# Performance work log

Measured on AMD Instinct MI355X. Metric: run time of the kernel, lower is better.

The kernel has to match this reference:

```python
import jax, jax.numpy as jnp
import numpy as np

N_NODES = 50000
NEG_SLOPE = 0.2  # PyG GATConv default
EPS = 1e-16      # PyG softmax eps


def gat_conv(x, src, dst, W, a_s, a_d, b, n_nodes):
    """One PyG-style GATConv layer (concat heads). a_s/a_d: [H, C]."""
    H, C = a_s.shape
    h = (x @ W).reshape(n_nodes, H, C)                   # [N, H, C]
    al_s = jnp.sum(h * a_s[None], axis=-1)               # [N, H]
    al_d = jnp.sum(h * a_d[None], axis=-1)               # [N, H]
    e = jax.nn.leaky_relu(al_s[src] + al_d[dst], NEG_SLOPE)  # [E, H]
    # segment softmax over incoming edges of each destination node
    m = jax.ops.segment_max(e, dst, num_segments=n_nodes)
    m = jnp.where(jnp.isfinite(m), m, 0.0)
    ex = jnp.exp(e - m[dst])
    denom = jax.ops.segment_sum(ex, dst, num_segments=n_nodes)
    alpha = ex / (denom[dst] + EPS)                       # [E, H]
    out = jax.ops.segment_sum(alpha[:, :, None] * h[src], dst, num_segments=n_nodes)
    return out.reshape(n_nodes, H * C) + b                # concat heads + bias


def setup_inputs() -> dict:
    key = jax.random.key(0)
    ks = jax.random.split(key, 16)
    s = 0.05
    return {
        "x": jax.random.normal(ks[0], (N_NODES, 256), jnp.float32),
        "edge_index": jax.random.randint(ks[1], (2, 800000), 0, N_NODES, jnp.int64),
        "W1": jax.random.normal(ks[2], (256, 256), jnp.float32) * s,
        "as1": jax.random.normal(ks[3], (4, 64), jnp.float32) * s,
        "ad1": jax.random.normal(ks[4], (4, 64), jnp.float32) * s,
        "b1": jnp.zeros((256,), jnp.float32),
        "W2": jax.random.normal(ks[5], (256, 256), jnp.float32) * s,
        "as2": jax.random.normal(ks[6], (4, 64), jnp.float32) * s,
        "ad2": jax.random.normal(ks[7], (4, 64), jnp.float32) * s,
        "b2": jnp.zeros((256,), jnp.float32),
        "W3": jax.random.normal(ks[8], (256, 128), jnp.float32) * s,
        "as3": jax.random.normal(ks[9], (1, 128), jnp.float32) * s,
        "ad3": jax.random.normal(ks[10], (1, 128), jnp.float32) * s,
        "b3": jnp.zeros((128,), jnp.float32),
    }


def reference(x, edge_index, W1, as1, ad1, b1, W2, as2, ad2, b2, W3, as3, ad3, b3):
    n = x.shape[0]
    loop = jnp.arange(n, dtype=edge_index.dtype)
    src = jnp.concatenate([edge_index[0], loop])  # add_self_loops=True (PyG default)
    dst = jnp.concatenate([edge_index[1], loop])
    # F.dropout(p=0.6, training=False) -> identity in eval
    h = gat_conv(x, src, dst, W1, as1, ad1, b1, n)
    h = jax.nn.elu(h)  # gnn_act='elu'
    h = gat_conv(h, src, dst, W2, as2, ad2, b2, n)
    h = jax.nn.elu(h)
    h = gat_conv(h, src, dst, W3, as3, ad3, b3, n)
    return h
```

## Files before the change

### kernel.cpp

```cpp
#include <hip/hip_runtime.h>
#include <math.h>


#define NEG_SLOPE 0.2f
#define EPS_SM 1e-16f

typedef _Float16 half8 __attribute__((ext_vector_type(8)));
typedef _Float16 half4v __attribute__((ext_vector_type(4)));
typedef _Float16 half2v __attribute__((ext_vector_type(2)));
typedef float f32x4 __attribute__((ext_vector_type(4)));

__device__ __forceinline__ float wave_allred_sum(float v) {
#pragma unroll
    for (int o = 32; o > 0; o >>= 1) v += __shfl_xor(v, o, 64);
    return v;
}
__device__ __forceinline__ float4 lrelu4(float4 v) {
    v.x = (v.x < 0.f) ? NEG_SLOPE * v.x : v.x;
    v.y = (v.y < 0.f) ? NEG_SLOPE * v.y : v.y;
    v.z = (v.z < 0.f) ? NEG_SLOPE * v.z : v.z;
    v.w = (v.w < 0.f) ? NEG_SLOPE * v.w : v.w;
    return v;
}

__global__ void build_fused(const int* __restrict__ ei, int E, int N, int nbE,
                            int* __restrict__ cnt, int* __restrict__ csr,
                            const float* __restrict__ W1,
                            const float* __restrict__ W2,
                            const float* __restrict__ W3,
                            const float* __restrict__ as1, const float* __restrict__ ad1,
                            const float* __restrict__ as2, const float* __restrict__ ad2,
                            const float* __restrict__ as3, const float* __restrict__ ad3,
                            _Float16* __restrict__ o1,
                            _Float16* __restrict__ o2,
                            _Float16* __restrict__ o3) {
    const int b = blockIdx.x;
    if (b < nbE) {
        int e = b * 256 + threadIdx.x;
        int ET = E + N;
        if (e >= ET) return;
        int src, dst;
        if (e < E) { src = ei[e]; dst = ei[E + e]; }
        else       { src = dst = e - E; }
        int slot = atomicAdd(&cnt[dst], 1);
        if (slot < 128) csr[(dst << 7) + slot] = src;
        return;
    }
    int i = (b - nbE) * 256 + threadIdx.x;
    if (i < 65536) {
        int n = i >> 8, k = i & 255;
        o1[i] = (_Float16)W1[(size_t)k * 256 + n];
    } else if (i < 131072) {
        int s = i - 65536; int n = s >> 8, k = s & 255;
        o2[s] = (_Float16)W2[(size_t)k * 256 + n];
    } else if (i < 163840) {
        int s = i - 131072; int n = s >> 8, k = s & 255;
        o3[s] = (_Float16)W3[(size_t)k * 128 + n];
    } else if (i < 163840 + 4096) {
        int t = i - 163840; int j = t >> 8, k = t & 255;
        float acc = 0.f;
        if (j < 8) {
            int h = j & 3;
            const float* a = ((j < 4) ? as1 : ad1) + h * 64;
            const float* wr = W1 + (size_t)k * 256 + h * 64;
            for (int c = 0; c < 64; ++c) acc += wr[c] * a[c];
        }
        o1[65536 + t] = (_Float16)acc;
    } else if (i < 163840 + 8192) {
        int t = i - 163840 - 4096; int j = t >> 8, k = t & 255;
        float acc = 0.f;
        if (j < 8) {
            int h = j & 3;
            const float* a = ((j < 4) ? as2 : ad2) + h * 64;
            const float* wr = W2 + (size_t)k * 256 + h * 64;
            for (int c = 0; c < 64; ++c) acc += wr[c] * a[c];
        }
        o2[65536 + t] = (_Float16)acc;
    } else if (i < 163840 + 12288) {
        int t = i - 163840 - 8192; int j = t >> 8, k = t & 255;
        float acc = 0.f;
        if (j < 2) {
            const float* a = (j == 0) ? as3 : ad3;
            const float* wr = W3 + (size_t)k * 128;
            for (int c = 0; c < 128; ++c) acc += wr[c] * a[c];
        }
        o3[32768 + t] = (_Float16)acc;
    }
}

template <bool AF32>
__global__ __launch_bounds__(256) void gemm_wide64(
    const void* __restrict__ Ain, const _Float16* __restrict__ Bt,
    _Float16* __restrict__ C,
    float* __restrict__ als, float* __restrict__ ald, int M) {
    const int K = 256, N = 256;
    __shared__ _Float16 As[2][64][40], Bs[2][272][40];
    const int bm = blockIdx.x * 64;
    const int tid = threadIdx.x;
    const int w = tid >> 6, lane = tid & 63;
    const int wn = w * 64;
    const int l16 = lane & 15, q = lane >> 4;
    const int kq = q * 8;
    const int arow = tid >> 2, ak = (tid & 3) * 8;
    const int brow = tid;
    const int agrow = bm + arow;
    const int NT = K >> 5;

    f32x4 acc[4][4], acce[4];
#pragma unroll
    for (int i = 0; i < 4; ++i) {
#pragma unroll
        for (int j = 0; j < 4; ++j) acc[i][j] = (f32x4){0.f, 0.f, 0.f, 0.f};
        acce[i] = (f32x4){0.f, 0.f, 0.f, 0.f};
    }

    half8 ra, rb0, rb1, rb2, rb3, rbe;
    auto LOAD = [&](int kt) {
        if constexpr (AF32) {
            const float* Af = (const float*)Ain;
            float4 v0, v1;
            if (agrow < M) {
                const float4* ap = (const float4*)(Af + (size_t)agrow * K + kt + ak);
                v0 = ap[0]; v1 = ap[1];
            } else {
                v0 = v1 = make_float4(0.f, 0.f, 0.f, 0.f);
            }
            ra[0] = (_Float16)v0.x; ra[1] = (_Float16)v0.y;
            ra[2] = (_Float16)v0.z; ra[3] = (_Float16)v0.w;
            ra[4] = (_Float16)v1.x; ra[5] = (_Float16)v1.y;
            ra[6] = (_Float16)v1.z; ra[7] = (_Float16)v1.w;
        } else {
            const _Float16* Ah = (const _Float16*)Ain;
            if (agrow < M) {
                ra = *(const half8*)(Ah + (size_t)agrow * K + kt + ak);
            } else {
                ra = (half8)(_Float16)0;
            }
        }
        const half8* bp = (const half8*)(Bt + (size_t)brow * K + kt);
        rb0 = bp[0]; rb1 = bp[1]; rb2 = bp[2]; rb3 = bp[3];
        if (tid < 64) {
            int er = tid >> 2, ek = (tid & 3) * 8;
            rbe = *(const half8*)(Bt + (size_t)(256 + er) * K + kt + ek);
        }
    };
    auto STORE = [&](int nb) {
        *(half8*)&As[nb][arow][ak]  = ra;
        *(half8*)&Bs[nb][brow][0]   = rb0;
        *(half8*)&Bs[nb][brow][8]   = rb1;
        *(half8*)&Bs[nb][brow][16]  = rb2;
        *(half8*)&Bs[nb][brow][24]  = rb3;
        if (tid < 64) {
            int er = tid >> 2, ek = (tid & 3) * 8;
            *(half8*)&Bs[nb][256 + er][ek] = rbe;
        }
    };

    LOAD(0);
    STORE(0);
    int cur = 0;
    for (int kb = 0; kb < NT; ++kb) {
        const bool more = (kb + 1) < NT;
        if (more) LOAD((kb + 1) * 32);
        __syncthreads();
        half8 a[4], b[4];
#pragma unroll
        for (int t = 0; t < 4; ++t) {
            a[t] = *(const half8*)&As[cur][t * 16 + l16][kq];
            b[t] = *(const half8*)&Bs[cur][wn + t * 16 + l16][kq];
        }
#pragma unroll
        for (int i = 0; i < 4; ++i)
#pragma unroll
            for (int j = 0; j < 4; ++j)
                acc[i][j] = __builtin_amdgcn_mfma_f32_16x16x32_f16(
                    a[i], b[j], acc[i][j], 0, 0, 0);
        if (w == 0) {
            half8 be = *(const half8*)&Bs[cur][256 + l16][kq];
#pragma unroll
            for (int i = 0; i < 4; ++i)
                acce[i] = __builtin_amdgcn_mfma_f32_16x16x32_f16(
                    a[i], be, acce[i], 0, 0, 0);
        }
        if (more) STORE(cur ^ 1);
        cur ^= 1;
    }

#pragma unroll
    for (int i = 0; i < 4; ++i) {
#pragma unroll
        for (int r = 0; r < 4; ++r) {
            int orow = bm + i * 16 + q * 4 + r;
            if (orow < M) {
                _Float16* cp = C + (size_t)orow * N + wn + l16;
                cp[0]  = (_Float16)acc[i][0][r];
                cp[16] = (_Float16)acc[i][1][r];
                cp[32] = (_Float16)acc[i][2][r];
                cp[48] = (_Float16)acc[i][3][r];
            }
        }
    }
    if (w == 0) {
#pragma unroll
        for (int i = 0; i < 4; ++i) {
#pragma unroll
            for (int r = 0; r < 4; ++r) {
                int orow = bm + i * 16 + q * 4 + r;
                if (orow < M) {
                    float c = acce[i][r];
                    if (l16 < 4)      als[orow * 4 + l16] = c;
                    else if (l16 < 8) ald[orow * 4 + (l16 - 4)] = c;
                }
            }
        }
    }
}

__global__ __launch_bounds__(256) void gemm_f16_l3(
    const _Float16* __restrict__ Ain, const _Float16* __restrict__ Bt,
    _Float16* __restrict__ C,
    float* __restrict__ als, float* __restrict__ ald,
    int M, int N, int K) {
    __shared__ _Float16 As[2][128][40], Bs[2][144][40];
    const int bm = blockIdx.y * 128;
    const int tid = threadIdx.x;
    const int w = tid >> 6, lane = tid & 63;
    const int wm = (w >> 1) * 64, wn = (w & 1) * 64;
    const int l16 = lane & 15, q = lane >> 4;
    const int kq = q * 8;
    const int sr = tid >> 1;
    const int sk = (tid & 1) * 16;
    const int row = bm + sr;
    const int NT = K >> 5;

    f32x4 acc[4][4], acce[4];
#pragma unroll
    for (int i = 0; i < 4; ++i) {
#pragma unroll
        for (int j = 0; j < 4; ++j) acc[i][j] = (f32x4){0.f, 0.f, 0.f, 0.f};
        acce[i] = (f32x4){0.f, 0.f, 0.f, 0.f};
    }

    half8 ra0, ra1, rb0, rb1, rbe;
    auto LOAD = [&](int kt) {
        if (row < M) {
            const half8* ap = (const half8*)(Ain + (size_t)row * K + kt + sk);
            ra0 = ap[0]; ra1 = ap[1];
        } else {
            ra0 = (half8)(_Float16)0; ra1 = (half8)(_Float16)0;
        }
        const half8* bp = (const half8*)(Bt + (size_t)sr * K + kt + sk);
        rb0 = bp[0]; rb1 = bp[1];
        if (tid < 64) {
            int er = tid >> 2, ek = (tid & 3) * 8;
            rbe = *(const half8*)(Bt + (size_t)(128 + er) * K + kt + ek);
        }
    };
    auto STORE = [&](int nb) {
        *(half8*)&As[nb][sr][sk]     = ra0;
        *(half8*)&As[nb][sr][sk + 8] = ra1;
        *(half8*)&Bs[nb][sr][sk]     = rb0;
        *(half8*)&Bs[nb][sr][sk + 8] = rb1;
        if (tid < 64) {
            int er = tid >> 2, ek = (tid & 3) * 8;
            *(half8*)&Bs[nb][128 + er][ek] = rbe;
        }
    };

    LOAD(0);
    STORE(0);
    int cur = 0;
    for (int kb = 0; kb < NT; ++kb) {
        const bool more = (kb + 1) < NT;
        if (more) LOAD((kb + 1) * 32);
        __syncthreads();
        half8 a[4], b[4];
#pragma unroll
        for (int t = 0; t < 4; ++t) {
            a[t] = *(const half8*)&As[cur][wm + t * 16 + l16][kq];
            b[t] = *(const half8*)&Bs[cur][wn + t * 16 + l16][kq];
        }
#pragma unroll
        for (int i = 0; i < 4; ++i)
#pragma unroll
            for (int j = 0; j < 4; ++j)
                acc[i][j] = __builtin_amdgcn_mfma_f32_16x16x32_f16(
                    a[i], b[j], acc[i][j], 0, 0, 0);
        if (wn == 0) {
            half8 be = *(const half8*)&Bs[cur][128 + l16][kq];
#pragma unroll
            for (int i = 0; i < 4; ++i)
                acce[i] = __builtin_amdgcn_mfma_f32_16x16x32_f16(
                    a[i], be, acce[i], 0, 0, 0);
        }
        if (more) STORE(cur ^ 1);
        cur ^= 1;
    }

#pragma unroll
    for (int i = 0; i < 4; ++i) {
#pragma unroll
        for (int r = 0; r < 4; ++r) {
            int orow = bm + wm + i * 16 + q * 4 + r;
            if (orow < M) {
                _Float16* cp = C + (size_t)orow * N + wn + l16;
                cp[0]  = (_Float16)acc[i][0][r];
                cp[16] = (_Float16)acc[i][1][r];
                cp[32] = (_Float16)acc[i][2][r];
                cp[48] = (_Float16)acc[i][3][r];
            }
        }
    }
    if (wn == 0) {
#pragma unroll
        for (int i = 0; i < 4; ++i) {
#pragma unroll
            for (int r = 0; r < 4; ++r) {
                int orow = bm + wm + i * 16 + q * 4 + r;
                if (orow < M) {
                    float c = acce[i][r];
                    if (l16 == 0)      als[orow] = c;
                    else if (l16 == 1) ald[orow] = c;
                }
            }
        }
    }
}

template <bool ACT>
__global__ __launch_bounds__(256) void aggregate_h4_f16(
    const _Float16* __restrict__ h, const float4* __restrict__ als4,
    const float4* __restrict__ ald4, const int* __restrict__ cnt,
    const int* __restrict__ csr, const float* __restrict__ bias,
    _Float16* __restrict__ out, int Nn) {
    const int tid = threadIdx.x;
    const int w = tid >> 6;
    const int l = tid & 63;
    const int n = blockIdx.x * 4 + w;
    __shared__ float s_alpha[4][64][4];
    __shared__ int s_src[4][64];
    if (n >= Nn) return;

    const int base = n << 7;
    const int deg = min(cnt[n], 128);
    const float4 adv = ald4[n];
    const int head = l >> 4;

    float4 acc = make_float4(0.f, 0.f, 0.f, 0.f);
    float4 den = make_float4(0.f, 0.f, 0.f, 0.f);
    for (int c0 = 0; c0 < deg; c0 += 64) {
        const int cl = min(64, deg - c0);
        if (l < cl) {
            int s = csr[base + c0 + l];
            float4 a = als4[s];
            float4 sc = lrelu4(make_float4(a.x + adv.x, a.y + adv.y,
                                           a.z + adv.z, a.w + adv.w));
            float4 ex = make_float4(__expf(sc.x), __expf(sc.y),
                                    __expf(sc.z), __expf(sc.w));
            *(float4*)&s_alpha[w][l][0] = ex;
            s_src[w][l] = s;
            den.x += ex.x; den.y += ex.y; den.z += ex.z; den.w += ex.w;
        }
        int e = 0;
        for (; e + 4 <= cl; e += 4) {
            int s0 = s_src[w][e + 0], s1 = s_src[w][e + 1];
            int s2 = s_src[w][e + 2], s3 = s_src[w][e + 3];
            float a0 = s_alpha[w][e + 0][head];
            float a1 = s_alpha[w][e + 1][head];
            float a2 = s_alpha[w][e + 2][head];
            float a3 = s_alpha[w][e + 3][head];
            half4v hv0 = *(const half4v*)(h + (size_t)s0 * 256 + l * 4);
            half4v hv1 = *(const half4v*)(h + (size_t)s1 * 256 + l * 4);
            half4v hv2 = *(const half4v*)(h + (size_t)s2 * 256 + l * 4);
            half4v hv3 = *(const half4v*)(h + (size_t)s3 * 256 + l * 4);
            acc.x = fmaf(a0, (float)hv0[0], acc.x);
            acc.y = fmaf(a0, (float)hv0[1], acc.y);
            acc.z = fmaf(a0, (float)hv0[2], acc.z);
            acc.w = fmaf(a0, (float)hv0[3], acc.w);
            acc.x = fmaf(a1, (float)hv1[0], acc.x);
            acc.y = fmaf(a1, (float)hv1[1], acc.y);
            acc.z = fmaf(a1, (float)hv1[2], acc.z);
            acc.w = fmaf(a1, (float)hv1[3], acc.w);
            acc.x = fmaf(a2, (float)hv2[0], acc.x);
            acc.y = fmaf(a2, (float)hv2[1], acc.y);
            acc.z = fmaf(a2, (float)hv2[2], acc.z);
            acc.w = fmaf(a2, (float)hv2[3], acc.w);
            acc.x = fmaf(a3, (float)hv3[0], acc.x);
            acc.y = fmaf(a3, (float)hv3[1], acc.y);
            acc.z = fmaf(a3, (float)hv3[2], acc.z);
            acc.w = fmaf(a3, (float)hv3[3], acc.w);
        }
        for (; e < cl; ++e) {
            int s0 = s_src[w][e];
            float a0 = s_alpha[w][e][head];
            half4v hv0 = *(const half4v*)(h + (size_t)s0 * 256 + l * 4);
            acc.x = fmaf(a0, (float)hv0[0], acc.x);
            acc.y = fmaf(a0, (float)hv0[1], acc.y);
            acc.z = fmaf(a0, (float)hv0[2], acc.z);
            acc.w = fmaf(a0, (float)hv0[3], acc.w);
        }
    }
    den.x = wave_allred_sum(den.x); den.y = wave_allred_sum(den.y);
    den.z = wave_allred_sum(den.z); den.w = wave_allred_sum(den.w);
    float d = (head == 0) ? den.x : (head == 1) ? den.y
             : (head == 2) ? den.z : den.w;
    const float rc = 1.f / (d + EPS_SM);

    float4 bv = *(const float4*)(bias + l * 4);
    float4 r = make_float4(acc.x * rc + bv.x, acc.y * rc + bv.y,
                           acc.z * rc + bv.z, acc.w * rc + bv.w);
    if (ACT) {
        r.x = (r.x > 0.f) ? r.x : expm1f(r.x);
        r.y = (r.y > 0.f) ? r.y : expm1f(r.y);
        r.z = (r.z > 0.f) ? r.z : expm1f(r.z);
        r.w = (r.w > 0.f) ? r.w : expm1f(r.w);
    }
    half4v ov = {(_Float16)r.x, (_Float16)r.y, (_Float16)r.z, (_Float16)r.w};
    *(half4v*)(out + (size_t)n * 256 + l * 4) = ov;
}

__global__ __launch_bounds__(256) void aggregate_h1_f16(
    const _Float16* __restrict__ h, const float* __restrict__ als,
    const float* __restrict__ ald, const int* __restrict__ cnt,
    const int* __restrict__ csr, const float* __restrict__ bias,
    float* __restrict__ out, int Nn) {
    const int tid = threadIdx.x;
    const int w = tid >> 6;
    const int l = tid & 63;
    const int n = blockIdx.x * 4 + w;
    __shared__ float s_alpha[4][64];
    __shared__ int s_src[4][64];
    if (n >= Nn) return;

    const int base = n << 7;
    const int deg = min(cnt[n], 128);
    const float ad_n = ald[n];

    float2 acc = make_float2(0.f, 0.f);
    float den = 0.f;
    for (int c0 = 0; c0 < deg; c0 += 64) {
        const int cl = min(64, deg - c0);
        if (l < cl) {
            int s = csr[base + c0 + l];
            float sc = als[s] + ad_n;
            sc = (sc < 0.f) ? NEG_SLOPE * sc : sc;
            float ex = __expf(sc);
            s_alpha[w][l] = ex;
            s_src[w][l] = s;
            den += ex;
        }
        int e = 0;
        for (; e + 4 <= cl; e += 4) {
            int s0 = s_src[w][e + 0], s1 = s_src[w][e + 1];
            int s2 = s_src[w][e + 2], s3 = s_src[w][e + 3];
            float a0 = s_alpha[w][e + 0], a1 = s_alpha[w][e + 1];
            float a2 = s_alpha[w][e + 2], a3 = s_alpha[w][e + 3];
            half2v v0 = *(const half2v*)(h + (size_t)s0 * 128 + l * 2);
            half2v v1 = *(const half2v*)(h + (size_t)s1 * 128 + l * 2);
            half2v v2 = *(const half2v*)(h + (size_t)s2 * 128 + l * 2);
            half2v v3 = *(const half2v*)(h + (size_t)s3 * 128 + l * 2);
            acc.x = fmaf(a0, (float)v0[0], acc.x); acc.y = fmaf(a0, (float)v0[1], acc.y);
            acc.x = fmaf(a1, (float)v1[0], acc.x); acc.y = fmaf(a1, (float)v1[1], acc.y);
            acc.x = fmaf(a2, (float)v2[0], acc.x); acc.y = fmaf(a2, (float)v2[1], acc.y);
            acc.x = fmaf(a3, (float)v3[0], acc.x); acc.y = fmaf(a3, (float)v3[1], acc.y);
        }
        for (; e < cl; ++e) {
            int s0 = s_src[w][e];
            float a0 = s_alpha[w][e];
            half2v v0 = *(const half2v*)(h + (size_t)s0 * 128 + l * 2);
            acc.x = fmaf(a0, (float)v0[0], acc.x); acc.y = fmaf(a0, (float)v0[1], acc.y);
        }
    }
    den = wave_allred_sum(den);
    const float rc = 1.f / (den + EPS_SM);
    float2 r = make_float2(acc.x * rc + bias[l * 2],
                           acc.y * rc + bias[l * 2 + 1]);
    *(float2*)(out + (size_t)n * 128 + l * 2) = r;
}

extern "C" void kernel_launch(void* const* d_in, const int* in_sizes, int n_in,
                              void* d_out, int out_size, void* d_ws,
                              size_t ws_size, hipStream_t stream) {
    const float* x   = (const float*)d_in[0];
    const int*   ei  = (const int*)d_in[1];
    const float* W1  = (const float*)d_in[2];
    const float* as1 = (const float*)d_in[3];
    const float* ad1 = (const float*)d_in[4];
    const float* b1  = (const float*)d_in[5];
    const float* W2  = (const float*)d_in[6];
    const float* as2 = (const float*)d_in[7];
    const float* ad2 = (const float*)d_in[8];
    const float* b2  = (const float*)d_in[9];
    const float* W3  = (const float*)d_in[10];
    const float* as3 = (const float*)d_in[11];
    const float* ad3 = (const float*)d_in[12];
    const float* b3  = (const float*)d_in[13];

    const int Nn = in_sizes[0] / 256;
    const int E  = in_sizes[1] / 2;
    const int ET = E + Nn;

    char* p = (char*)d_ws;
    _Float16* bufA = (_Float16*)p; p += (size_t)Nn * 256 * 2;
    _Float16* bufB = (_Float16*)p; p += (size_t)Nn * 256 * 2;
    float* als  = (float*)p; p += (size_t)Nn * 4 * 4;
    float* ald  = (float*)p; p += (size_t)Nn * 4 * 4;
    int* cnt  = (int*)p; p += (size_t)Nn * 4;
    int* csr  = (int*)p; p += (size_t)Nn * 128 * 4;
    p = (char*)(((uintptr_t)p + 15) & ~(uintptr_t)15);
    _Float16* wt1 = (_Float16*)p; p += 272 * 256 * 2;
    _Float16* wt2 = (_Float16*)p; p += 272 * 256 * 2;
    _Float16* wt3 = (_Float16*)p; p += 144 * 256 * 2;

    hipMemsetAsync(cnt, 0, (size_t)Nn * sizeof(int), stream);
    const int nbE = (ET + 255) / 256;
    const int nbW = (163840 + 12288 + 255) / 256;
    build_fused<<<nbE + nbW, 256, 0, stream>>>(
        ei, E, Nn, nbE, cnt, csr,
        W1, W2, W3, as1, ad1, as2, ad2, as3, ad3, wt1, wt2, wt3);

    const int gm64 = (Nn + 63) / 64;
    const int gm   = (Nn + 127) / 128;
    const int ga   = (Nn + 3) / 4;

    gemm_wide64<true><<<gm64, 256, 0, stream>>>(
        x, wt1, bufB, als, ald, Nn);
    aggregate_h4_f16<true><<<ga, 256, 0, stream>>>(
        bufB, (const float4*)als, (const float4*)ald, cnt, csr, b1, bufA, Nn);

    gemm_wide64<false><<<gm64, 256, 0, stream>>>(
        bufA, wt2, bufB, als, ald, Nn);
    aggregate_h4_f16<true><<<ga, 256, 0, stream>>>(
        bufB, (const float4*)als, (const float4*)ald, cnt, csr, b2, bufA, Nn);

    gemm_f16_l3<<<dim3(1, gm), 256, 0, stream>>>(
        bufA, wt3, bufB, als, ald, Nn, 128, 256);
    aggregate_h1_f16<<<ga, 256, 0, stream>>>(
        bufB, als, ald, cnt, csr, b3, (float*)d_out, Nn);
}
```

Measured before the change: 392.8 us.

## Fold CSR build into first GEMM launch and zero counters in prep kernel

Replaces the memset with a counter-zeroing section in the weight-prep kernel. The edge-bucketing atomics move out of that kernel and into extra blocks appended to the layer-1 GEMM grid, so CSR construction runs concurrently with the first GEMM. This removes one API call and hides the atomic scatter behind GEMM compute. The cost is that GEMM blocks share the device with the atomic-heavy blocks, and the build blocks still reserve the GEMM's shared-memory footprint, which may lower occupancy for them.

```diff
diff --git a/kernel.cpp b/kernel.cpp
--- a/kernel.cpp
+++ b/kernel.cpp
@@ -23,30 +23,23 @@
     return v;
 }
 
-__global__ void build_fused(const int* __restrict__ ei, int E, int N, int nbE,
-                            int* __restrict__ cnt, int* __restrict__ csr,
-                            const float* __restrict__ W1,
-                            const float* __restrict__ W2,
-                            const float* __restrict__ W3,
-                            const float* __restrict__ as1, const float* __restrict__ ad1,
-                            const float* __restrict__ as2, const float* __restrict__ ad2,
-                            const float* __restrict__ as3, const float* __restrict__ ad3,
-                            _Float16* __restrict__ o1,
-                            _Float16* __restrict__ o2,
-                            _Float16* __restrict__ o3) {
+__global__ void prep(int* __restrict__ cnt, int Nn, int nbZ,
+                     const float* __restrict__ W1,
+                     const float* __restrict__ W2,
+                     const float* __restrict__ W3,
+                     const float* __restrict__ as1, const float* __restrict__ ad1,
+                     const float* __restrict__ as2, const float* __restrict__ ad2,
+                     const float* __restrict__ as3, const float* __restrict__ ad3,
+                     _Float16* __restrict__ o1,
+                     _Float16* __restrict__ o2,
+                     _Float16* __restrict__ o3) {
     const int b = blockIdx.x;
-    if (b < nbE) {
-        int e = b * 256 + threadIdx.x;
-        int ET = E + N;
-        if (e >= ET) return;
-        int src, dst;
-        if (e < E) { src = ei[e]; dst = ei[E + e]; }
-        else       { src = dst = e - E; }
-        int slot = atomicAdd(&cnt[dst], 1);
-        if (slot < 128) csr[(dst << 7) + slot] = src;
+    if (b < nbZ) {
+        int i = b * 256 + threadIdx.x;
+        if (i < Nn) cnt[i] = 0;
         return;
     }
-    int i = (b - nbE) * 256 + threadIdx.x;
+    int i = (b - nbZ) * 256 + threadIdx.x;
     if (i < 65536) {
         int n = i >> 8, k = i & 255;
         o1[i] = (_Float16)W1[(size_t)k * 256 + n];
@@ -88,13 +81,29 @@
     }
 }
 
-template <bool AF32>
+template <bool AF32, bool BUILD>
 __global__ __launch_bounds__(256) void gemm_wide64(
     const void* __restrict__ Ain, const _Float16* __restrict__ Bt,
     _Float16* __restrict__ C,
-    float* __restrict__ als, float* __restrict__ ald, int M) {
+    float* __restrict__ als, float* __restrict__ ald, int M,
+    const int* __restrict__ ei, int E,
+    int* __restrict__ cnt, int* __restrict__ csr, int nbG) {
     const int K = 256, N = 256;
     __shared__ _Float16 As[2][64][40], Bs[2][272][40];
+    if constexpr (BUILD) {
+        if (blockIdx.x >= nbG) {
+            int e = (blockIdx.x - nbG) * 256 + threadIdx.x;
+            int ET = E + M;
+            if (e < ET) {
+                int src, dst;
+                if (e < E) { src = ei[e]; dst = ei[E + e]; }
+                else       { src = dst = e - E; }
+                int slot = atomicAdd(&cnt[dst], 1);
+                if (slot < 128) csr[(dst << 7) + slot] = src;
+            }
+            return;
+        }
+    }
     const int bm = blockIdx.x * 64;
     const int tid = threadIdx.x;
     const int w = tid >> 6, lane = tid & 63;
@@ -512,24 +521,23 @@
     _Float16* wt2 = (_Float16*)p; p += 272 * 256 * 2;
     _Float16* wt3 = (_Float16*)p; p += 144 * 256 * 2;
 
-    hipMemsetAsync(cnt, 0, (size_t)Nn * sizeof(int), stream);
+    const int nbZ = (Nn + 255) / 256;
+    const int nbW = (163840 + 12288 + 255) / 256;
     const int nbE = (ET + 255) / 256;
-    const int nbW = (163840 + 12288 + 255) / 256;
-    build_fused<<<nbE + nbW, 256, 0, stream>>>(
-        ei, E, Nn, nbE, cnt, csr,
-        W1, W2, W3, as1, ad1, as2, ad2, as3, ad3, wt1, wt2, wt3);
-
     const int gm64 = (Nn + 63) / 64;
     const int gm   = (Nn + 127) / 128;
     const int ga   = (Nn + 3) / 4;
 
-    gemm_wide64<true><<<gm64, 256, 0, stream>>>(
-        x, wt1, bufB, als, ald, Nn);
+    prep<<<nbZ + nbW, 256, 0, stream>>>(
+        cnt, Nn, nbZ, W1, W2, W3, as1, ad1, as2, ad2, as3, ad3, wt1, wt2, wt3);
+
+    gemm_wide64<true, true><<<gm64 + nbE, 256, 0, stream>>>(
+        x, wt1, bufB, als, ald, Nn, ei, E, cnt, csr, gm64);
     aggregate_h4_f16<true><<<ga, 256, 0, stream>>>(
         bufB, (const float4*)als, (const float4*)ald, cnt, csr, b1, bufA, Nn);
 
-    gemm_wide64<false><<<gm64, 256, 0, stream>>>(
-        bufA, wt2, bufB, als, ald, Nn);
+    gemm_wide64<false, false><<<gm64, 256, 0, stream>>>(
+        bufA, wt2, bufB, als, ald, Nn, nullptr, 0, nullptr, nullptr, gm64);
     aggregate_h4_f16<true><<<ga, 256, 0, stream>>>(
         bufB, (const float4*)als, (const float4*)ald, cnt, csr, b2, bufA, Nn);
 
```

New measurement: 377.4 us. -3.9%, faster.

## Fuse all GAT stages into one persistent cooperative kernel with grid syncs

Applied to the files above, without the earlier changes.

Replaces the memset plus seven separate kernel launches with a single cooperative persistent kernel. The stages run in grid-stride loops over virtual blocks and are separated by grid.sync(). The first GEMM now overlaps with CSR construction in the same phase, and the counter zeroing moves into the prep phase. This removes per-launch overhead and inter-kernel gaps. In exchange it uses a fixed 53 KB shared buffer for every phase, which can lower occupancy, adds grid-wide barrier cost, and assumes 256 CUs when sizing the grid.

```diff
diff --git a/kernel.cpp b/kernel.cpp
--- a/kernel.cpp
+++ b/kernel.cpp
@@ -1,5 +1,8 @@
 #include <hip/hip_runtime.h>
+#include <hip/hip_cooperative_groups.h>
 #include <math.h>
+
+namespace cg = cooperative_groups;
 
 
 #define NEG_SLOPE 0.2f
@@ -9,6 +12,11 @@
 typedef _Float16 half4v __attribute__((ext_vector_type(4)));
 typedef _Float16 half2v __attribute__((ext_vector_type(2)));
 typedef float f32x4 __attribute__((ext_vector_type(4)));
+
+typedef _Float16 As64T[64][40];
+typedef _Float16 Bs272T[272][40];
+typedef _Float16 As128T[128][40];
+typedef _Float16 Bs144T[144][40];
 
 __device__ __forceinline__ float wave_allred_sum(float v) {
 #pragma unroll
@@ -23,79 +31,85 @@
     return v;
 }
 
-__global__ void build_fused(const int* __restrict__ ei, int E, int N, int nbE,
-                            int* __restrict__ cnt, int* __restrict__ csr,
-                            const float* __restrict__ W1,
-                            const float* __restrict__ W2,
-                            const float* __restrict__ W3,
-                            const float* __restrict__ as1, const float* __restrict__ ad1,
-                            const float* __restrict__ as2, const float* __restrict__ ad2,
-                            const float* __restrict__ as3, const float* __restrict__ ad3,
-                            _Float16* __restrict__ o1,
-                            _Float16* __restrict__ o2,
-                            _Float16* __restrict__ o3) {
-    const int b = blockIdx.x;
-    if (b < nbE) {
-        int e = b * 256 + threadIdx.x;
-        int ET = E + N;
-        if (e >= ET) return;
-        int src, dst;
-        if (e < E) { src = ei[e]; dst = ei[E + e]; }
-        else       { src = dst = e - E; }
-        int slot = atomicAdd(&cnt[dst], 1);
-        if (slot < 128) csr[(dst << 7) + slot] = src;
+struct GP {
+    const float* x; const int* ei;
+    const float *W1, *as1, *ad1, *b1;
+    const float *W2, *as2, *ad2, *b2;
+    const float *W3, *as3, *ad3, *b3;
+    _Float16 *bufA, *bufB, *wt1, *wt2, *wt3;
+    float *als, *ald;
+    int *cnt, *csr;
+    float* out;
+    int Nn, E;
+};
+
+__device__ __forceinline__ void prep_work(int vb, int nbZ, const GP& p) {
+    if (vb < nbZ) {
+        int i = vb * 256 + threadIdx.x;
+        if (i < p.Nn) p.cnt[i] = 0;
         return;
     }
-    int i = (b - nbE) * 256 + threadIdx.x;
+    int i = (vb - nbZ) * 256 + threadIdx.x;
     if (i < 65536) {
         int n = i >> 8, k = i & 255;
-        o1[i] = (_Float16)W1[(size_t)k * 256 + n];
+        p.wt1[i] = (_Float16)p.W1[(size_t)k * 256 + n];
     } else if (i < 131072) {
         int s = i - 65536; int n = s >> 8, k = s & 255;
-        o2[s] = (_Float16)W2[(size_t)k * 256 + n];
+        p.wt2[s] = (_Float16)p.W2[(size_t)k * 256 + n];
     } else if (i < 163840) {
         int s = i - 131072; int n = s >> 8, k = s & 255;
-        o3[s] = (_Float16)W3[(size_t)k * 128 + n];
+        p.wt3[s] = (_Float16)p.W3[(size_t)k * 128 + n];
     } else if (i < 163840 + 4096) {
         int t = i - 163840; int j = t >> 8, k = t & 255;
         float acc = 0.f;
         if (j < 8) {
             int h = j & 3;
-            const float* a = ((j < 4) ? as1 : ad1) + h * 64;
-            const float* wr = W1 + (size_t)k * 256 + h * 64;
+            const float* a = ((j < 4) ? p.as1 : p.ad1) + h * 64;
+            const float* wr = p.W1 + (size_t)k * 256 + h * 64;
             for (int c = 0; c < 64; ++c) acc += wr[c] * a[c];
         }
-        o1[65536 + t] = (_Float16)acc;
+        p.wt1[65536 + t] = (_Float16)acc;
     } else if (i < 163840 + 8192) {
         int t = i - 163840 - 4096; int j = t >> 8, k = t & 255;
         float acc = 0.f;
         if (j < 8) {
             int h = j & 3;
-            const float* a = ((j < 4) ? as2 : ad2) + h * 64;
-            const float* wr = W2 + (size_t)k * 256 + h * 64;
+            const float* a = ((j < 4) ? p.as2 : p.ad2) + h * 64;
+            const float* wr = p.W2 + (size_t)k * 256 + h * 64;
             for (int c = 0; c < 64; ++c) acc += wr[c] * a[c];
         }
-        o2[65536 + t] = (_Float16)acc;
+        p.wt2[65536 + t] = (_Float16)acc;
     } else if (i < 163840 + 12288) {
         int t = i - 163840 - 8192; int j = t >> 8, k = t & 255;
         float acc = 0.f;
         if (j < 2) {
-            const float* a = (j == 0) ? as3 : ad3;
-            const float* wr = W3 + (size_t)k * 128;
+            const float* a = (j == 0) ? p.as3 : p.ad3;
+            const float* wr = p.W3 + (size_t)k * 128;
             for (int c = 0; c < 128; ++c) acc += wr[c] * a[c];
         }
-        o3[32768 + t] = (_Float16)acc;
-    }
+        p.wt3[32768 + t] = (_Float16)acc;
+    }
+}
+
+__device__ __forceinline__ void build_work(int c, const GP& p) {
+    int e = c * 256 + threadIdx.x;
+    int ET = p.E + p.Nn;
+    if (e >= ET) return;
+    int src, dst;
+    if (e < p.E) { src = p.ei[e]; dst = p.ei[p.E + e]; }
+    else         { src = dst = e - p.E; }
+    int slot = atomicAdd(&p.cnt[dst], 1);
+    if (slot < 128) p.csr[(dst << 7) + slot] = src;
 }
 
 template <bool AF32>
-__global__ __launch_bounds__(256) void gemm_wide64(
-    const void* __restrict__ Ain, const _Float16* __restrict__ Bt,
-    _Float16* __restrict__ C,
-    float* __restrict__ als, float* __restrict__ ald, int M) {
+__device__ __forceinline__ void gemm64_tile(
+    char* smem, int vb, const void* Ain, const _Float16* Bt, _Float16* C,
+    float* als, float* ald, int M) {
     const int K = 256, N = 256;
-    __shared__ _Float16 As[2][64][40], Bs[2][272][40];
-    const int bm = blockIdx.x * 64;
+    As64T* As = (As64T*)smem;
+    Bs272T* Bs = (Bs272T*)(smem + 10240);
+    const int bm = vb * 64;
     const int tid = threadIdx.x;
     const int w = tid >> 6, lane = tid & 63;
     const int wn = w * 64;
@@ -216,13 +230,13 @@
     }
 }
 
-__global__ __launch_bounds__(256) void gemm_f16_l3(
-    const _Float16* __restrict__ Ain, const _Float16* __restrict__ Bt,
-    _Float16* __restrict__ C,
-    float* __restrict__ als, float* __restrict__ ald,
-    int M, int N, int K) {
-    __shared__ _Float16 As[2][128][40], Bs[2][144][40];
-    const int bm = blockIdx.y * 128;
+__device__ __forceinline__ void gemm3_tile(
+    char* smem, int vb, const _Float16* Ain, const _Float16* Bt, _Float16* C,
+    float* als, float* ald, int M) {
+    const int N = 128, K = 256;
+    As128T* As = (As128T*)smem;
+    Bs144T* Bs = (Bs144T*)(smem + 20480);
+    const int bm = vb * 128;
     const int tid = threadIdx.x;
     const int w = tid >> 6, lane = tid & 63;
     const int wm = (w >> 1) * 64, wn = (w & 1) * 64;
@@ -328,17 +342,16 @@
 }
 
 template <bool ACT>
-__global__ __launch_bounds__(256) void aggregate_h4_f16(
-    const _Float16* __restrict__ h, const float4* __restrict__ als4,
-    const float4* __restrict__ ald4, const int* __restrict__ cnt,
-    const int* __restrict__ csr, const float* __restrict__ bias,
-    _Float16* __restrict__ out, int Nn) {
+__device__ __forceinline__ void agg4_work(
+    char* smem, int vb, const _Float16* h, const float4* als4,
+    const float4* ald4, const int* cnt, const int* csr, const float* bias,
+    _Float16* out, int Nn) {
+    float (*s_alpha)[64][4] = (float(*)[64][4])smem;
+    int (*s_src)[64] = (int(*)[64])(smem + 4096);
     const int tid = threadIdx.x;
     const int w = tid >> 6;
     const int l = tid & 63;
-    const int n = blockIdx.x * 4 + w;
-    __shared__ float s_alpha[4][64][4];
-    __shared__ int s_src[4][64];
+    const int n = vb * 4 + w;
     if (n >= Nn) return;
 
     const int base = n << 7;
@@ -419,17 +432,16 @@
     *(half4v*)(out + (size_t)n * 256 + l * 4) = ov;
 }
 
-__global__ __launch_bounds__(256) void aggregate_h1_f16(
-    const _Float16* __restrict__ h, const float* __restrict__ als,
-    const float* __restrict__ ald, const int* __restrict__ cnt,
-    const int* __restrict__ csr, const float* __restrict__ bias,
-    float* __restrict__ out, int Nn) {
+__device__ __forceinline__ void agg1_work(
+    char* smem, int vb, const _Float16* h, const float* als,
+    const float* ald, const int* cnt, const int* csr, const float* bias,
+    float* out, int Nn) {
+    float (*s_alpha)[64] = (float(*)[64])smem;
+    int (*s_src)[64] = (int(*)[64])(smem + 1024);
     const int tid = threadIdx.x;
     const int w = tid >> 6;
     const int l = tid & 63;
-    const int n = blockIdx.x * 4 + w;
-    __shared__ float s_alpha[4][64];
-    __shared__ int s_src[4][64];
+    const int n = vb * 4 + w;
     if (n >= Nn) return;
 
     const int base = n << 7;
@@ -478,63 +490,91 @@
     *(float2*)(out + (size_t)n * 128 + l * 2) = r;
 }
 
+__global__ __launch_bounds__(256) void mega(GP p) {
+    cg::grid_group grid = cg::this_grid();
+    __shared__ __align__(16) char smem[53760];
+
+    const int nbZ = (p.Nn + 255) >> 8;
+    const int nbW = (163840 + 12288 + 255) >> 8;
+    const int nbE = (p.E + p.Nn + 255) >> 8;
+    const int gm64 = (p.Nn + 63) >> 6;
+    const int gm = (p.Nn + 127) >> 7;
+    const int ga = (p.Nn + 3) >> 2;
+
+    for (int vb = blockIdx.x; vb < nbZ + nbW; vb += gridDim.x)
+        prep_work(vb, nbZ, p);
+    grid.sync();
+    for (int vb = blockIdx.x; vb < gm64 + nbE; vb += gridDim.x) {
+        if (vb < gm64)
+            gemm64_tile<true>(smem, vb, p.x, p.wt1, p.bufB, p.als, p.ald, p.Nn);
+        else
+            build_work(vb - gm64, p);
+    }
+    grid.sync();
+    for (int vb = blockIdx.x; vb < ga; vb += gridDim.x)
+        agg4_work<true>(smem, vb, p.bufB, (const float4*)p.als,
+                        (const float4*)p.ald, p.cnt, p.csr, p.b1, p.bufA, p.Nn);
+    grid.sync();
+    for (int vb = blockIdx.x; vb < gm64; vb += gridDim.x)
+        gemm64_tile<false>(smem, vb, p.bufA, p.wt2, p.bufB, p.als, p.ald, p.Nn);
+    grid.sync();
+    for (int vb = blockIdx.x; vb < ga; vb += gridDim.x)
+        agg4_work<true>(smem, vb, p.bufB, (const float4*)p.als,
+                        (const float4*)p.ald, p.cnt, p.csr, p.b2, p.bufA, p.Nn);
+    grid.sync();
+    for (int vb = blockIdx.x; vb < gm; vb += gridDim.x)
+        gemm3_tile(smem, vb, p.bufA, p.wt3, p.bufB, p.als, p.ald, p.Nn);
+    grid.sync();
+    for (int vb = blockIdx.x; vb < ga; vb += gridDim.x)
+        agg1_work(smem, vb, p.bufB, p.als, p.ald, p.cnt, p.csr, p.b3,
+                  p.out, p.Nn);
+}
+
 extern "C" void kernel_launch(void* const* d_in, const int* in_sizes, int n_in,
                               void* d_out, int out_size, void* d_ws,
                               size_t ws_size, hipStream_t stream) {
-    const float* x   = (const float*)d_in[0];
-    const int*   ei  = (const int*)d_in[1];
-    const float* W1  = (const float*)d_in[2];
-    const float* as1 = (const float*)d_in[3];
-    const float* ad1 = (const float*)d_in[4];
-    const float* b1  = (const float*)d_in[5];
-    const float* W2  = (const float*)d_in[6];
-    const float* as2 = (const float*)d_in[7];
-    const float* ad2 = (const float*)d_in[8];
-    const float* b2  = (const float*)d_in[9];
-    const float* W3  = (const float*)d_in[10];
-    const float* as3 = (const float*)d_in[11];
-    const float* ad3 = (const float*)d_in[12];
-    const float* b3  = (const float*)d_in[13];
-
-    const int Nn = in_sizes[0] / 256;
-    const int E  = in_sizes[1] / 2;
-    const int ET = E + Nn;
-
-    char* p = (char*)d_ws;
-    _Float16* bufA = (_Float16*)p; p += (size_t)Nn * 256 * 2;
-    _Float16* bufB = (_Float16*)p; p += (size_t)Nn * 256 * 2;
-    float* als  = (float*)p; p += (size_t)Nn * 4 * 4;
-    float* ald  = (float*)p; p += (size_t)Nn * 4 * 4;
-    int* cnt  = (int*)p; p += (size_t)Nn * 4;
-    int* csr  = (int*)p; p += (size_t)Nn * 128 * 4;
-    p = (char*)(((uintptr_t)p + 15) & ~(uintptr_t)15);
-    _Float16* wt1 = (_Float16*)p; p += 272 * 256 * 2;
-    _Float16* wt2 = (_Float16*)p; p += 272 * 256 * 2;
-    _Float16* wt3 = (_Float16*)p; p += 144 * 256 * 2;
-
-    hipMemsetAsync(cnt, 0, (size_t)Nn * sizeof(int), stream);
-    const int nbE = (ET + 255) / 256;
-    const int nbW = (163840 + 12288 + 255) / 256;
-    build_fused<<<nbE + nbW, 256, 0, stream>>>(
-        ei, E, Nn, nbE, cnt, csr,
-        W1, W2, W3, as1, ad1, as2, ad2, as3, ad3, wt1, wt2, wt3);
-
-    const int gm64 = (Nn + 63) / 64;
-    const int gm   = (Nn + 127) / 128;
-    const int ga   = (Nn + 3) / 4;
-
-    gemm_wide64<true><<<gm64, 256, 0, stream>>>(
-        x, wt1, bufB, als, ald, Nn);
-    aggregate_h4_f16<true><<<ga, 256, 0, stream>>>(
-        bufB, (const float4*)als, (const float4*)ald, cnt, csr, b1, bufA, Nn);
-
-    gemm_wide64<false><<<gm64, 256, 0, stream>>>(
-        bufA, wt2, bufB, als, ald, Nn);
-    aggregate_h4_f16<true><<<ga, 256, 0, stream>>>(
-        bufB, (const float4*)als, (const float4*)ald, cnt, csr, b2, bufA, Nn);
-
-    gemm_f16_l3<<<dim3(1, gm), 256, 0, stream>>>(
-        bufA, wt3, bufB, als, ald, Nn, 128, 256);
-    aggregate_h1_f16<<<ga, 256, 0, stream>>>(
-        bufB, als, ald, cnt, csr, b3, (float*)d_out, Nn);
-}
+    GP p;
+    p.x   = (const float*)d_in[0];
+    p.ei  = (const int*)d_in[1];
+    p.W1  = (const float*)d_in[2];
+    p.as1 = (const float*)d_in[3];
+    p.ad1 = (const float*)d_in[4];
+    p.b1  = (const float*)d_in[5];
+    p.W2  = (const float*)d_in[6];
+    p.as2 = (const float*)d_in[7];
+    p.ad2 = (const float*)d_in[8];
+    p.b2  = (const float*)d_in[9];
+    p.W3  = (const float*)d_in[10];
+    p.as3 = (const float*)d_in[11];
+    p.ad3 = (const float*)d_in[12];
+    p.b3  = (const float*)d_in[13];
+    p.out = (float*)d_out;
+
+    p.Nn = in_sizes[0] / 256;
+    p.E  = in_sizes[1] / 2;
+
+    char* q = (char*)d_ws;
+    p.bufA = (_Float16*)q; q += (size_t)p.Nn * 256 * 2;
+    p.bufB = (_Float16*)q; q += (size_t)p.Nn * 256 * 2;
+    p.als  = (float*)q; q += (size_t)p.Nn * 4 * 4;
+    p.ald  = (float*)q; q += (size_t)p.Nn * 4 * 4;
+    p.cnt  = (int*)q; q += (size_t)p.Nn * 4;
+    p.csr  = (int*)q; q += (size_t)p.Nn * 128 * 4;
+    q = (char*)(((uintptr_t)q + 15) & ~(uintptr_t)15);
+    p.wt1 = (_Float16*)q; q += 272 * 256 * 2;
+    p.wt2 = (_Float16*)q; q += 272 * 256 * 2;
+    p.wt3 = (_Float16*)q; q += 144 * 256 * 2;
+
+    static int s_grid = 0;
+    if (s_grid == 0) {
+        int maxb = 0;
+        hipOccupancyMaxActiveBlocksPerMultiprocessor(&maxb, mega, 256, 0);
+        if (maxb < 1) maxb = 1;
+        s_grid = maxb * 256;
+        if (s_grid > 2048) s_grid = 2048;
+    }
+
+    void* args[] = {&p};
+    hipLaunchCooperativeKernel((void*)mega, dim3(s_grid), dim3(256),
+                               args, 0, stream);
+}
```

Result: slower. 962.4 us (+145.0%).
